# Kernel optimization log

Hardware: AMD Instinct MI355X
Metric: run time of the kernel (lower is better)

## Reference

```python
import jax, jax.numpy as jnp
import numpy as np

N_NODES = 50000
N_EDGES = 800000
IN_DIM = 128
OUT_DIM = 128
N_CLASSES = 10
N_GRAPHS = 64


def setup_inputs() -> dict:
    key = jax.random.key(0)
    ks = jax.random.split(key, 8)
    features = jax.random.normal(ks[0], (N_NODES, IN_DIM), dtype=jnp.float32)
    src = jax.random.randint(ks[1], (N_EDGES,), 0, N_NODES, dtype=jnp.int64)
    dst = jax.random.randint(ks[2], (N_EDGES,), 0, N_NODES, dtype=jnp.int64)
    graph_ids = jnp.sort(jax.random.randint(ks[3], (N_NODES,), 0, N_GRAPHS, dtype=jnp.int64))
    # GraphConv params (glorot-ish scale) and linear head params
    W = jax.random.normal(ks[4], (IN_DIM, OUT_DIM), dtype=jnp.float32) / np.sqrt(IN_DIM)
    b = jnp.zeros((OUT_DIM,), dtype=jnp.float32)
    W_head = jax.random.normal(ks[5], (OUT_DIM, N_CLASSES), dtype=jnp.float32) / np.sqrt(OUT_DIM)
    b_head = jnp.zeros((N_CLASSES,), dtype=jnp.float32)
    return {"features": features, "src": src, "dst": dst, "graph_ids": graph_ids,
            "W": W, "b": b, "W_head": W_head, "b_head": b_head}


def reference(features, src, dst, graph_ids, W, b, W_head, b_head):
    # DGL GraphConv, norm='both': D_out^-1/2 -> sum aggregate -> D_in^-1/2 -> XW+b -> relu
    ones_e = jnp.ones((src.shape[0],), dtype=features.dtype)
    out_deg = jax.ops.segment_sum(ones_e, src, num_segments=N_NODES)
    in_deg = jax.ops.segment_sum(ones_e, dst, num_segments=N_NODES)
    out_norm = jax.lax.rsqrt(jnp.clip(out_deg, 1.0))[:, None]   # [N,1]
    in_norm = jax.lax.rsqrt(jnp.clip(in_deg, 1.0))[:, None]     # [N,1]
    h = features * out_norm                                      # [N,D]
    agg = jax.ops.segment_sum(h[src], dst, num_segments=N_NODES) # gather-scatter [E,D]->[N,D]
    agg = agg * in_norm
    h = jax.nn.relu(agg @ W + b)                                 # [N,D_out]
    # dgl.mean_nodes: segment mean over graphs (note: original returns after layer 0)
    cnt = jax.ops.segment_sum(jnp.ones((N_NODES,), dtype=h.dtype), graph_ids, num_segments=N_GRAPHS)
    pooled = jax.ops.segment_sum(h, graph_ids, num_segments=N_GRAPHS) / jnp.clip(cnt, 1.0)[:, None]
    return pooled @ W_head + b_head                              # [G, n_classes]
```

## Files before the change

kernel.cpp:

```cpp
#include <hip/hip_runtime.h>

#define N_NODES   50000
#define N_EDGES   800000
#define DIM       128
#define N_GRAPHS  64
#define N_CLASSES 10
#define CAP       64
#define NCHE      64
#define CSZ       (N_EDGES / NCHE)
#define LQ        (N_NODES / 4)
#define WPB       64
#define NBR2      ((LQ + WPB - 1) / WPB)
#define PLACE_BPC ((CSZ + 255) / 256)
#define PLACE_BLKS (NCHE * PLACE_BPC)
#define PRES_BLKS ((N_NODES * DIM / 8 + 255) / 256)
#define K3_BLKS   (PLACE_BLKS + PRES_BLKS)
#define WT_BLKS   (DIM * DIM / 256)
#define GS_BLKS   ((N_NODES + 255) / 256)
#define LH_HIST   (2 * NCHE)
#define K1_BLKS   (LH_HIST + WT_BLKS + GS_BLKS)
#define NPBM      128
#define NBLK_NODE ((N_NODES + NPBM - 1) / NPBM)

typedef _Float16 h8 __attribute__((ext_vector_type(8)));
typedef float f4v __attribute__((ext_vector_type(4)));

#define RSQN(D) rsqrtf(fmaxf((float)(D), 1.0f))

__global__ __launch_bounds__(256) void k_pre(const int* __restrict__ src,
                                             const int* __restrict__ dst,
                                             unsigned* __restrict__ Hin,
                                             unsigned* __restrict__ Hout,
                                             unsigned char* __restrict__ perm,
                                             const float* __restrict__ W,
                                             _Float16* __restrict__ Wt,
                                             const int* __restrict__ gid,
                                             int* __restrict__ gstart,
                                             const float* __restrict__ bh,
                                             float* __restrict__ out) {
    __shared__ unsigned L[LQ];
    int blk = blockIdx.x, t = threadIdx.x;
    if (blk >= LH_HIST) {
        int q = blk - LH_HIST;
        if (q < WT_BLKS) {
            int i = q * 256 + t;
            int n = i >> 7, k = i & 127;
            Wt[n * DIM + k] = (_Float16)W[k * DIM + n];
            if (i < N_GRAPHS * N_CLASSES) out[i] = bh[i % N_CLASSES];
        } else {
            int i = (q - WT_BLKS) * 256 + t;
            if (i < N_NODES) {
                int gq = gid[i];
                if (i == 0) {
                    for (int x = 0; x <= gq; ++x) gstart[x] = 0;
                } else {
                    int gp = gid[i - 1];
                    if (gp != gq)
                        for (int x = gp + 1; x <= gq; ++x) gstart[x] = i;
                }
                if (i == N_NODES - 1)
                    for (int x = gq + 1; x <= N_GRAPHS; ++x) gstart[x] = N_NODES;
            }
        }
        return;
    }
    int c = blk & (NCHE - 1);
    int phase = blk >> 6;
    int base = c * CSZ;
    for (int w = t; w < LQ; w += 256) L[w] = 0u;
    __syncthreads();
    if (phase == 0) {
        for (int i = t; i < CSZ; i += 256) {
            int d = dst[base + i];
            int sh = (d & 3) * 8;
            unsigned old = atomicAdd(&L[d >> 2], 1u << sh);
            perm[base + i] = (unsigned char)((old >> sh) & 0xffu);
        }
        __syncthreads();
        for (int w = t; w < LQ; w += 256) Hin[(size_t)c * LQ + w] = L[w];
    } else {
        for (int i = t; i < CSZ; i += 256) {
            int s = src[base + i];
            atomicAdd(&L[s >> 2], 1u << ((s & 3) * 8));
        }
        __syncthreads();
        for (int w = t; w < LQ; w += 256) Hout[(size_t)c * LQ + w] = L[w];
    }
}

__global__ __launch_bounds__(256) void k_reduce(unsigned* __restrict__ Hin,
                                                const unsigned* __restrict__ Hout,
                                                unsigned* __restrict__ indeg,
                                                unsigned* __restrict__ outdeg) {
    __shared__ unsigned sIn[4][WPB];
    __shared__ unsigned sOut[4][WPB];
    int t = threadIdx.x;
    int wl = t & (WPB - 1);
    int g  = t >> 6;
    int w  = blockIdx.x * WPB + wl;
    unsigned gs = 0, os = 0;
    int c0 = g * (NCHE / 4);
    if (w < LQ) {
        for (int c = c0; c < c0 + NCHE / 4; ++c) {
            gs += Hin[(size_t)c * LQ + w];
            os += Hout[(size_t)c * LQ + w];
        }
    }
    sIn[g][wl] = gs; sOut[g][wl] = os;
    __syncthreads();
    unsigned baseg = 0;
    for (int gg = 0; gg < 4; ++gg) if (gg < g) baseg += sIn[gg][wl];
    if (w < LQ) {
        unsigned running = baseg;
        for (int c = c0; c < c0 + NCHE / 4; ++c) {
            size_t idx = (size_t)c * LQ + w;
            unsigned word = Hin[idx];
            Hin[idx] = running;
            running += word;
        }
    }
    __syncthreads();
    if (t < WPB) {
        int ww = blockIdx.x * WPB + t;
        if (ww < LQ) {
            unsigned tot  = sIn[0][t] + sIn[1][t] + sIn[2][t] + sIn[3][t];
            unsigned otot = sOut[0][t] + sOut[1][t] + sOut[2][t] + sOut[3][t];
            int n = 4 * ww;
            indeg[n]      = tot & 0xffu;
            indeg[n + 1]  = (tot >> 8) & 0xffu;
            indeg[n + 2]  = (tot >> 16) & 0xffu;
            indeg[n + 3]  = tot >> 24;
            outdeg[n]     = otot & 0xffu;
            outdeg[n + 1] = (otot >> 8) & 0xffu;
            outdeg[n + 2] = (otot >> 16) & 0xffu;
            outdeg[n + 3] = otot >> 24;
        }
    }
}

__global__ __launch_bounds__(256) void k_place(const int* __restrict__ src,
                                               const int* __restrict__ dst,
                                               const unsigned* __restrict__ Hin,
                                               const unsigned char* __restrict__ perm,
                                               unsigned short* __restrict__ bsrc,
                                               const float* __restrict__ feat,
                                               const unsigned* __restrict__ outdeg,
                                               _Float16* __restrict__ sfeat) {
    int t = threadIdx.x;
    int blk = blockIdx.x;
    if (blk < PLACE_BLKS) {
        int c = blk / PLACE_BPC;
        int i = (blk % PLACE_BPC) * 256 + t;
        if (i < CSZ) {
            int e = c * CSZ + i;
            int d = dst[e];
            int sh = (d & 3) * 8;
            unsigned pre = (Hin[(size_t)c * LQ + (d >> 2)] >> sh) & 0xffu;
            unsigned slot = pre + perm[e];
            if (slot < CAP) bsrc[(size_t)d * CAP + slot] = (unsigned short)src[e];
        }
    } else {
        int i = (blk - PLACE_BLKS) * 256 + t;
        if (i < N_NODES * DIM / 8) {
            int n = i >> 4;
            float nrm = RSQN(outdeg[n]);
            const float4* p = reinterpret_cast<const float4*>(feat + (size_t)i * 8);
            float4 a = p[0], qv = p[1];
            h8 r;
            r[0] = (_Float16)(a.x * nrm);  r[1] = (_Float16)(a.y * nrm);
            r[2] = (_Float16)(a.z * nrm);  r[3] = (_Float16)(a.w * nrm);
            r[4] = (_Float16)(qv.x * nrm); r[5] = (_Float16)(qv.y * nrm);
            r[6] = (_Float16)(qv.z * nrm); r[7] = (_Float16)(qv.w * nrm);
            *reinterpret_cast<h8*>(sfeat + (size_t)i * 8) = r;
        }
    }
}

__device__ __forceinline__ h8 shfl_down_h8(h8 v, int d) {
    union { h8 h; int i[4]; } u;
    u.h = v;
    u.i[0] = __shfl_down(u.i[0], d);
    u.i[1] = __shfl_down(u.i[1], d);
    u.i[2] = __shfl_down(u.i[2], d);
    u.i[3] = __shfl_down(u.i[3], d);
    return u.h;
}

__global__ __launch_bounds__(256) void k_gather(const unsigned short* __restrict__ bsrc,
                                                const unsigned* __restrict__ indeg,
                                                const _Float16* __restrict__ sfeat,
                                                _Float16* __restrict__ aggh) {
    int tid = threadIdx.x;
    int wave = tid >> 6;
    int lane = tid & 63;
    int node = blockIdx.x * 4 + wave;
    if (node >= N_NODES) return;
    unsigned start = (unsigned)node * CAP;
    unsigned deg   = indeg[node];
    unsigned lim   = deg < (unsigned)CAP ? deg : (unsigned)CAP;
    int qtr = lane >> 4;
    int d8  = (lane & 15) << 3;
    int sIdx = 0;
    if ((unsigned)lane < lim) sIdx = bsrc[start + lane];
    h8 accA = (h8)(_Float16)0.f;
    h8 accC = (h8)(_Float16)0.f;
    for (unsigned j = 0; j < lim; j += 16) {
        unsigned j0 = j + qtr, j1 = j + 4 + qtr, j2 = j + 8 + qtr, j3 = j + 12 + qtr;
        int s0 = __shfl(sIdx, (int)(j0 < lim ? j0 : 0u));
        int s1 = __shfl(sIdx, (int)(j1 < lim ? j1 : 0u));
        int s2 = __shfl(sIdx, (int)(j2 < lim ? j2 : 0u));
        int s3 = __shfl(sIdx, (int)(j3 < lim ? j3 : 0u));
        _Float16 m0 = (j0 < lim) ? (_Float16)1.f : (_Float16)0.f;
        _Float16 m1 = (j1 < lim) ? (_Float16)1.f : (_Float16)0.f;
        _Float16 m2 = (j2 < lim) ? (_Float16)1.f : (_Float16)0.f;
        _Float16 m3 = (j3 < lim) ? (_Float16)1.f : (_Float16)0.f;
        h8 r0 = *reinterpret_cast<const h8*>(sfeat + (size_t)s0 * DIM + d8);
        h8 r1 = *reinterpret_cast<const h8*>(sfeat + (size_t)s1 * DIM + d8);
        h8 r2 = *reinterpret_cast<const h8*>(sfeat + (size_t)s2 * DIM + d8);
        h8 r3 = *reinterpret_cast<const h8*>(sfeat + (size_t)s3 * DIM + d8);
        accA += r0 * m0;
        accC += r1 * m1;
        accA += r2 * m2;
        accC += r3 * m3;
    }
    accA += accC;
    accA += shfl_down_h8(accA, 32);
    accA += shfl_down_h8(accA, 16);
    if (qtr == 0) {
        float innrm = RSQN(deg);
        h8 r;
#pragma unroll
        for (int k = 0; k < 8; ++k) r[k] = (_Float16)((float)accA[k] * innrm);
        *reinterpret_cast<h8*>(aggh + (size_t)node * DIM + d8) = r;
    }
}

__global__ __launch_bounds__(256) void k_node(const _Float16* __restrict__ aggh,
                                              const int* __restrict__ gid,
                                              const _Float16* __restrict__ Wt,
                                              const float* __restrict__ b,
                                              const float* __restrict__ Wh,
                                              const int* __restrict__ gstart,
                                              float* __restrict__ out) {
    __shared__ float red[4][2][DIM];
    __shared__ float vb[2][DIM];
    int tid = threadIdx.x;
    int wave = tid >> 6, lane = tid & 63;
    int quad = lane >> 4, m = lane & 15;
    int blockBase = blockIdx.x * NPBM;
    int wbase = blockBase + wave * 32;
    int gfirst = gid[blockBase];
    int gsec = gfirst + 1;

    f4v acc0[8], acc1[8];
#pragma unroll
    for (int t = 0; t < 8; ++t) { acc0[t] = (f4v){0,0,0,0}; acc1[t] = (f4v){0,0,0,0}; }

#pragma unroll
    for (int kk = 0; kk < 4; ++kk) {
        int ko = kk * 32 + quad * 8;
        h8 a0 = *reinterpret_cast<const h8*>(aggh + (size_t)(wbase + m) * DIM + ko);
        h8 a1 = *reinterpret_cast<const h8*>(aggh + (size_t)(wbase + 16 + m) * DIM + ko);
#pragma unroll
        for (int t = 0; t < 8; ++t) {
            h8 bf = *reinterpret_cast<const h8*>(Wt + (size_t)(t * 16 + m) * DIM + ko);
            acc0[t] = __builtin_amdgcn_mfma_f32_16x16x32_f16(a0, bf, acc0[t], 0, 0, 0);
            acc1[t] = __builtin_amdgcn_mfma_f32_16x16x32_f16(a1, bf, acc1[t], 0, 0, 0);
        }
    }

    int n0 = wbase + quad * 4;
    int n1 = n0 + 16;
    float s0[8], s1[8];
#pragma unroll
    for (int t = 0; t < 8; ++t) {
        float bb = b[t * 16 + m];
        s0[t] = 0.f; s1[t] = 0.f;
        int dimIdx = t * 16 + m;
#pragma unroll
        for (int r = 0; r < 4; ++r) {
            int node = n0 + r;
            if (node < N_NODES) {
                float h = fmaxf(acc0[t][r] + bb, 0.f);
                int g = gid[node];
                if (g == gfirst)      s0[t] += h;
                else if (g == gsec)   s1[t] += h;
                else {
                    float cntg = fmaxf((float)(gstart[g + 1] - gstart[g]), 1.f);
                    float hw = h / cntg;
                    for (int c = 0; c < N_CLASSES; ++c)
                        atomicAdd(&out[g * N_CLASSES + c], hw * Wh[dimIdx * N_CLASSES + c]);
                }
            }
            int node2 = n1 + r;
            if (node2 < N_NODES) {
                float h = fmaxf(acc1[t][r] + bb, 0.f);
                int g = gid[node2];
                if (g == gfirst)      s0[t] += h;
                else if (g == gsec)   s1[t] += h;
                else {
                    float cntg = fmaxf((float)(gstart[g + 1] - gstart[g]), 1.f);
                    float hw = h / cntg;
                    for (int c = 0; c < N_CLASSES; ++c)
                        atomicAdd(&out[g * N_CLASSES + c], hw * Wh[dimIdx * N_CLASSES + c]);
                }
            }
        }
        s0[t] += __shfl_down(s0[t], 32);
        s0[t] += __shfl_down(s0[t], 16);
        s1[t] += __shfl_down(s1[t], 32);
        s1[t] += __shfl_down(s1[t], 16);
    }
    if (quad == 0) {
#pragma unroll
        for (int t = 0; t < 8; ++t) {
            red[wave][0][t * 16 + m] = s0[t];
            red[wave][1][t * 16 + m] = s1[t];
        }
    }
    __syncthreads();
    if (tid < DIM) {
        vb[0][tid] = red[0][0][tid] + red[1][0][tid] + red[2][0][tid] + red[3][0][tid];
        vb[1][tid] = red[0][1][tid] + red[1][1][tid] + red[2][1][tid] + red[3][1][tid];
    }
    __syncthreads();
    if (tid < N_CLASSES) {
        int c = tid;
        float s = 0.f;
#pragma unroll 8
        for (int k = 0; k < DIM; ++k) s += vb[0][k] * Wh[k * N_CLASSES + c];
        if (s != 0.f) {
            float cnt = fmaxf((float)(gstart[gfirst + 1] - gstart[gfirst]), 1.f);
            atomicAdd(&out[gfirst * N_CLASSES + c], s / cnt);
        }
    } else if (tid >= 64 && tid < 64 + N_CLASSES && gsec < N_GRAPHS) {
        int c = tid - 64;
        float s = 0.f;
#pragma unroll 8
        for (int k = 0; k < DIM; ++k) s += vb[1][k] * Wh[k * N_CLASSES + c];
        if (s != 0.f) {
            float cnt = fmaxf((float)(gstart[gsec + 1] - gstart[gsec]), 1.f);
            atomicAdd(&out[gsec * N_CLASSES + c], s / cnt);
        }
    }
}

extern "C" void kernel_launch(void* const* d_in, const int* in_sizes, int n_in,
                              void* d_out, int out_size, void* d_ws, size_t ws_size,
                              hipStream_t stream) {
    const float* feat = (const float*)d_in[0];
    const int*   src  = (const int*)d_in[1];
    const int*   dst  = (const int*)d_in[2];
    const int*   gid  = (const int*)d_in[3];
    const float* W    = (const float*)d_in[4];
    const float* b    = (const float*)d_in[5];
    const float* Wh   = (const float*)d_in[6];
    const float* bh   = (const float*)d_in[7];
    float* out = (float*)d_out;

    unsigned* indeg    = (unsigned*)d_ws;
    unsigned* outdeg   = indeg + N_NODES;
    int*      gstart   = (int*)(outdeg + N_NODES);
    unsigned short* bsrc = (unsigned short*)(gstart + 128);
    _Float16* sfeat    = (_Float16*)(bsrc + (size_t)N_NODES * CAP);
    _Float16* aggh     = sfeat + (size_t)N_NODES * DIM;
    _Float16* Wt       = aggh + (size_t)N_NODES * DIM;
    unsigned* Hin      = (unsigned*)(Wt + DIM * DIM);
    unsigned* Hout     = Hin + (size_t)NCHE * LQ;
    unsigned char* perm= (unsigned char*)(Hout + (size_t)NCHE * LQ);

    k_pre   <<<K1_BLKS, 256, 0, stream>>>(src, dst, Hin, Hout, perm,
                                          W, Wt, gid, gstart, bh, out);
    k_reduce<<<NBR2, 256, 0, stream>>>(Hin, Hout, indeg, outdeg);
    k_place <<<K3_BLKS, 256, 0, stream>>>(src, dst, Hin, perm, bsrc,
                                          feat, outdeg, sfeat);
    k_gather<<<(N_NODES + 3) / 4, 256, 0, stream>>>(bsrc, indeg, sfeat, aggh);
    k_node  <<<NBLK_NODE, 256, 0, stream>>>(aggh, gid, Wt, b, Wh, gstart, out);
}
```

Before: 166.5 us.

## Stage transposed weights in padded LDS and halve nodes per block

The node kernel now copies the fp16 transposed weight matrix into shared memory with a padded row stride, so the MFMA B operands are read from LDS instead of global memory. Each wave now handles 16 nodes instead of 32, so blocks cover 64 nodes and there are twice as many blocks. This removes repeated global/L2 weight reads but adds a 32KB-per-block LDS staging step and a barrier. With half the nodes per block, that staging cost is spread over less work.

```diff
diff --git a/kernel.cpp b/kernel.cpp
--- a/kernel.cpp
+++ b/kernel.cpp
@@ -19,8 +19,9 @@
 #define GS_BLKS   ((N_NODES + 255) / 256)
 #define LH_HIST   (2 * NCHE)
 #define K1_BLKS   (LH_HIST + WT_BLKS + GS_BLKS)
-#define NPBM      128
+#define NPBM      64
 #define NBLK_NODE ((N_NODES + NPBM - 1) / NPBM)
+#define WPAD      136
 
 typedef _Float16 h8 __attribute__((ext_vector_type(8)));
 typedef float f4v __attribute__((ext_vector_type(4)));
@@ -242,35 +243,40 @@
                                               const float* __restrict__ Wh,
                                               const int* __restrict__ gstart,
                                               float* __restrict__ out) {
+    __shared__ _Float16 Lw[DIM * WPAD];
     __shared__ float red[4][2][DIM];
     __shared__ float vb[2][DIM];
     int tid = threadIdx.x;
     int wave = tid >> 6, lane = tid & 63;
     int quad = lane >> 4, m = lane & 15;
     int blockBase = blockIdx.x * NPBM;
-    int wbase = blockBase + wave * 32;
+    int wbase = blockBase + wave * 16;
     int gfirst = gid[blockBase];
     int gsec = gfirst + 1;
 
-    f4v acc0[8], acc1[8];
-#pragma unroll
-    for (int t = 0; t < 8; ++t) { acc0[t] = (f4v){0,0,0,0}; acc1[t] = (f4v){0,0,0,0}; }
+    for (int i = tid; i < DIM * DIM / 8; i += 256) {
+        int n = i >> 4, k8 = i & 15;
+        h8 v = *reinterpret_cast<const h8*>(Wt + (size_t)n * DIM + k8 * 8);
+        *reinterpret_cast<h8*>(&Lw[n * WPAD + k8 * 8]) = v;
+    }
+    __syncthreads();
+
+    f4v acc[8];
+#pragma unroll
+    for (int t = 0; t < 8; ++t) acc[t] = (f4v){0,0,0,0};
 
 #pragma unroll
     for (int kk = 0; kk < 4; ++kk) {
         int ko = kk * 32 + quad * 8;
         h8 a0 = *reinterpret_cast<const h8*>(aggh + (size_t)(wbase + m) * DIM + ko);
-        h8 a1 = *reinterpret_cast<const h8*>(aggh + (size_t)(wbase + 16 + m) * DIM + ko);
 #pragma unroll
         for (int t = 0; t < 8; ++t) {
-            h8 bf = *reinterpret_cast<const h8*>(Wt + (size_t)(t * 16 + m) * DIM + ko);
-            acc0[t] = __builtin_amdgcn_mfma_f32_16x16x32_f16(a0, bf, acc0[t], 0, 0, 0);
-            acc1[t] = __builtin_amdgcn_mfma_f32_16x16x32_f16(a1, bf, acc1[t], 0, 0, 0);
+            h8 bf = *reinterpret_cast<const h8*>(&Lw[(t * 16 + m) * WPAD + ko]);
+            acc[t] = __builtin_amdgcn_mfma_f32_16x16x32_f16(a0, bf, acc[t], 0, 0, 0);
         }
     }
 
     int n0 = wbase + quad * 4;
-    int n1 = n0 + 16;
     float s0[8], s1[8];
 #pragma unroll
     for (int t = 0; t < 8; ++t) {
@@ -281,21 +287,8 @@
         for (int r = 0; r < 4; ++r) {
             int node = n0 + r;
             if (node < N_NODES) {
-                float h = fmaxf(acc0[t][r] + bb, 0.f);
+                float h = fmaxf(acc[t][r] + bb, 0.f);
                 int g = gid[node];
-                if (g == gfirst)      s0[t] += h;
-                else if (g == gsec)   s1[t] += h;
-                else {
-                    float cntg = fmaxf((float)(gstart[g + 1] - gstart[g]), 1.f);
-                    float hw = h / cntg;
-                    for (int c = 0; c < N_CLASSES; ++c)
-                        atomicAdd(&out[g * N_CLASSES + c], hw * Wh[dimIdx * N_CLASSES + c]);
-                }
-            }
-            int node2 = n1 + r;
-            if (node2 < N_NODES) {
-                float h = fmaxf(acc1[t][r] + bb, 0.f);
-                int g = gid[node2];
                 if (g == gfirst)      s0[t] += h;
                 else if (g == gsec)   s1[t] += h;
                 else {
```

Result: faster. 159.2 us (-4.4%).
